# Kernel optimization log

Measured on AMD Instinct MI355X. Metric: run time of the kernel, lower is better.

The kernel has to match this reference:

```python
import jax, jax.numpy as jnp
import numpy as np

EMBED_DIM = 256
NUM_HEADS = 8
QUERY_HEAD_DIM = 24
BLOCK_SIZE = 8
IN_PROJ_DIM = 2 * QUERY_HEAD_DIM * NUM_HEADS  # 384


def _relative_position_index(bs: int) -> np.ndarray:
    coords = np.stack(np.meshgrid(np.arange(bs), np.arange(bs), indexing='ij'))  # (2, bs, bs)
    cf = coords.reshape(2, -1)                          # (2, bs^2)
    rel = cf[:, :, None] - cf[:, None, :]               # (2, bs^2, bs^2)
    rel = rel.transpose(1, 2, 0).astype(np.int32)       # (bs^2, bs^2, 2)
    rel[..., 0] += bs - 1
    rel[..., 1] += bs - 1
    rel[..., 0] *= 2 * bs - 1
    return rel.sum(-1)                                  # (bs^2, bs^2)


def setup_inputs() -> dict:
    key = jax.random.key(0)
    k1, k2, k3, k4, k5 = jax.random.split(key, 5)
    B, H, W, C = 2, 256, 256, EMBED_DIM
    num_tokens = H * W
    x = jax.random.normal(k1, (B, H, W, C), dtype=jnp.float32)
    reordered_indexes = jax.random.randint(k2, (1, num_tokens, 1), 0, num_tokens).astype(jnp.int64)
    # ScaledLinear: ordinary linear; initial_scale folded into weight magnitude
    scale = QUERY_HEAD_DIM ** (-0.25)
    w_in = jax.random.normal(k3, (EMBED_DIM, IN_PROJ_DIM), dtype=jnp.float32) * (scale / np.sqrt(EMBED_DIM))
    b_in = jax.random.normal(k4, (IN_PROJ_DIM,), dtype=jnp.float32) * 0.01
    n_rel = (2 * BLOCK_SIZE - 1) ** 2
    rel_bias_table = jax.random.uniform(k5, (n_rel, NUM_HEADS), dtype=jnp.float32) * 0.02
    rel_pos_index = jnp.asarray(_relative_position_index(BLOCK_SIZE), dtype=jnp.int32)
    return {"x": x, "reordered_indexes": reordered_indexes, "w_in": w_in,
            "b_in": b_in, "rel_bias_table": rel_bias_table, "rel_pos_index": rel_pos_index}


def reference(x, reordered_indexes, w_in, b_in, rel_bias_table, rel_pos_index):
    B, H, W, C = x.shape
    bs = BLOCK_SIZE
    nh = NUM_HEADS
    qhd = QUERY_HEAD_DIM
    nbh, nbw = H // bs, W // bs
    nbt = nbh * nbw
    num_tokens = H * W

    # optional token reordering (gather along token dim)
    idx = reordered_indexes[0, :, 0]                        # (num_tokens,)
    xf = x.reshape(B, num_tokens, C)[:, idx, :]             # (B, T, C)
    xf = xf.reshape(B, H, W, C)

    proj = xf @ w_in + b_in                                 # (B, H, W, 2*nh*qhd)
    qdim = qhd * nh
    query = proj[..., :qdim]
    key = proj[..., qdim:2 * qdim]  # whiten/balance are identity in eval math

    # window partition: (B, nbh, bs, nbw, bs, nh, qhd)
    q = query.reshape(B, nbh, bs, nbw, bs, nh, qhd)
    q = q.transpose(5, 0, 1, 3, 2, 4, 6).reshape(nh, B, nbt, bs * bs, qhd)
    k = key.reshape(B, nbh, bs, nbw, bs, nh, qhd)
    k = k.transpose(5, 0, 1, 3, 6, 2, 4).reshape(nh, B, nbt, qhd, bs * bs)

    attn_scores = jnp.matmul(q, k)                          # (nh, B, nbt, bs^2, bs^2)

    bias = rel_bias_table[rel_pos_index.reshape(-1)]        # (bs^2*bs^2, nh)
    bias = bias.reshape(bs * bs, bs * bs, nh).transpose(2, 0, 1)  # (nh, bs^2, bs^2)
    attn_scores = attn_scores + bias[:, None, None]

    return jax.nn.softmax(attn_scores, axis=-1)
```

## Files before the change

kernel.cpp:

```cpp
#include <hip/hip_runtime.h>

namespace {

typedef __attribute__((ext_vector_type(4))) float f32x4;
typedef __attribute__((ext_vector_type(8))) short bf16x8;

constexpr int WFRAG_ELEMS = 24 * 8 * 64 * 8;
constexpr int WFRAG_BYTES = WFRAG_ELEMS * 2;
constexpr int BIAS_ELEMS  = 8 * 64 * 64;
constexpr size_t WS_NEEDED = (size_t)WFRAG_BYTES + (size_t)BIAS_ELEMS * 4;

constexpr int TOK_OFF = 0;
constexpr int XS_OFF  = 256;
constexpr int CB_OFF  = 0;
constexpr int PB_OFF  = 49152;
constexpr int LDS_TOTAL = 65536;

__device__ __forceinline__ unsigned short f2bf(float f) {
  unsigned u = __float_as_uint(f);
  u += 0x7fffu + ((u >> 16) & 1u);
  return (unsigned short)(u >> 16);
}

__device__ __forceinline__ int cb_addr(int row, int col) {
  const int slot = (col >> 3) ^ (row & 7);
  return CB_OFF + row * 768 + (slot << 4) + ((col & 7) << 1);
}

__device__ __forceinline__ int pb_addr(int wavebase, int row16, int ktq) {
  return wavebase + row16 * 256 + (((ktq ^ row16) & 15) << 4);
}

__global__ void prep(const float* __restrict__ w_in,
                     const float* __restrict__ btab,
                     const int*   __restrict__ rpidx,
                     unsigned short* __restrict__ wfrag,
                     float* __restrict__ biasx) {
  const int t = blockIdx.x * 256 + threadIdx.x;
  if (t < WFRAG_ELEMS) {
    const int j    = t & 7;
    const int lane = (t >> 3) & 63;
    const int kk   = (t >> 9) & 7;
    const int nt   = t >> 12;
    const int k    = kk * 32 + (lane >> 4) * 8 + j;
    const int col  = nt * 16 + (lane & 15);
    wfrag[t] = f2bf(w_in[k * 384 + col]);
  } else if (t < WFRAG_ELEMS + BIAS_ELEMS) {
    const int o = t - WFRAG_ELEMS;
    const int j = o & 63, i = (o >> 6) & 63, h = o >> 12;
    biasx[o] = btab[rpidx[i * 64 + j] * 8 + h];
  }
}

template <bool USE_WS>
__global__ __launch_bounds__(256, 2)
void fused_mhaw(const float* __restrict__ x,
                const int*   __restrict__ reidx,
                const float* __restrict__ w_in,
                const float* __restrict__ b_in,
                const float* __restrict__ btab,
                const int*   __restrict__ rpidx,
                const unsigned short* __restrict__ wfrag,
                const float* __restrict__ biasx,
                float*       __restrict__ out) {
  extern __shared__ char lds[];
  int* tok           = reinterpret_cast<int*>(lds + TOK_OFF);
  unsigned short* xs = reinterpret_cast<unsigned short*>(lds + XS_OFF);

  const int tid  = threadIdx.x;
  const int b    = blockIdx.x >> 10;
  const int win  = blockIdx.x & 1023;
  const int wh   = win >> 5, ww = win & 31;
  const int wave = tid >> 6, lane = tid & 63;
  const int l15  = lane & 15, q = lane >> 4;
  const int pbase = PB_OFF + wave * 4096;

  if (tid < 64)
    tok[tid] = reidx[(wh * 8 + (tid >> 3)) * 256 + ww * 8 + (tid & 7)];
  __syncthreads();

  {
    const int srow = tid >> 2;
    const int part = tid & 3;
    const int sm_t = srow >> 4, sr15 = srow & 15;
    const int swr  = sr15 ^ (part << 1);
    const float* xrow = x + ((size_t)b * 65536 + (size_t)tok[srow]) * 256;
#pragma unroll
    for (int hf = 0; hf < 2; ++hf) {
      const float* src = xrow + hf * 128 + part * 32;
#pragma unroll
      for (int g = 0; g < 4; ++g) {
        const float4 v0 = *reinterpret_cast<const float4*>(src + g * 8);
        const float4 v1 = *reinterpret_cast<const float4*>(src + g * 8 + 4);
        bf16x8 u;
        u[0] = (short)f2bf(v0.x); u[1] = (short)f2bf(v0.y);
        u[2] = (short)f2bf(v0.z); u[3] = (short)f2bf(v0.w);
        u[4] = (short)f2bf(v1.x); u[5] = (short)f2bf(v1.y);
        u[6] = (short)f2bf(v1.z); u[7] = (short)f2bf(v1.w);
        *reinterpret_cast<bf16x8*>(
            xs + ((sm_t * 8 + hf * 4 + part) * 64 + g * 16 + swr) * 8) = u;
      }
    }
  }
  __syncthreads();

  f32x4 acc[6][4];
#pragma unroll
  for (int n = 0; n < 6; ++n)
#pragma unroll
    for (int m = 0; m < 4; ++m) acc[n][m] = (f32x4){0.f, 0.f, 0.f, 0.f};

#pragma unroll
  for (int kk = 0; kk < 8; ++kk) {
    const int rlane = q * 16 + (l15 ^ ((kk & 3) << 1));
    bf16x8 af[4];
#pragma unroll
    for (int m = 0; m < 4; ++m)
      af[m] = *reinterpret_cast<const bf16x8*>(xs + ((m * 8 + kk) * 64 + rlane) * 8);
#pragma unroll
    for (int n = 0; n < 6; ++n) {
      bf16x8 bfr;
      if (USE_WS) {
        bfr = *reinterpret_cast<const bf16x8*>(
            wfrag + (((wave * 6 + n) * 8 + kk) * 64 + lane) * 8);
      } else {
        const int colg = wave * 96 + n * 16 + l15;
#pragma unroll
        for (int jj = 0; jj < 8; ++jj)
          bfr[jj] = (short)f2bf(w_in[(kk * 32 + q * 8 + jj) * 384 + colg]);
      }
#pragma unroll
      for (int m = 0; m < 4; ++m)
        acc[n][m] = __builtin_amdgcn_mfma_f32_16x16x32_bf16(af[m], bfr, acc[n][m], 0, 0, 0);
    }
  }
  __syncthreads();

#pragma unroll
  for (int n = 0; n < 6; ++n) {
    const int colg = wave * 96 + n * 16 + l15;
    const float bv = b_in[colg];
#pragma unroll
    for (int m = 0; m < 4; ++m)
#pragma unroll
      for (int r = 0; r < 4; ++r) {
        const int row = m * 16 + q * 4 + r;
        *reinterpret_cast<unsigned short*>(lds + cb_addr(row, colg)) =
            f2bf(acc[n][m][r] + bv);
      }
  }
  __syncthreads();

  const bf16x8 vz = {0, 0, 0, 0, 0, 0, 0, 0};
  const f32x4 cz = {0.f, 0.f, 0.f, 0.f};

  for (int hh = 0; hh < 2; ++hh) {
    const int h = wave * 2 + hh;

    bf16x8 aq[4], bk[4];
#pragma unroll
    for (int mi = 0; mi < 4; ++mi)
      aq[mi] = (lane < 48)
                   ? *reinterpret_cast<const bf16x8*>(lds + cb_addr(mi * 16 + l15, h * 24 + q * 8))
                   : vz;
#pragma unroll
    for (int ni = 0; ni < 4; ++ni)
      bk[ni] = (lane < 48)
                   ? *reinterpret_cast<const bf16x8*>(lds + cb_addr(ni * 16 + l15, 192 + h * 24 + q * 8))
                   : vz;

    f32x4 s[4][4];
#pragma unroll
    for (int ai = 0; ai < 4; ++ai)
#pragma unroll
      for (int bi = 0; bi < 4; ++bi)
        s[ai][bi] = __builtin_amdgcn_mfma_f32_16x16x32_bf16(bk[ai], aq[bi], cz, 0, 0, 0);

    const size_t obase = (((size_t)h * 2 + b) * 1024 + win) * 4096;

#pragma unroll
    for (int bi = 0; bi < 4; ++bi) {
      const int qt = bi * 16 + l15;
      f32x4 p[4];
#pragma unroll
      for (int ai = 0; ai < 4; ++ai) {
        if (USE_WS) {
          const f32x4 bb = *reinterpret_cast<const f32x4*>(
              biasx + ((size_t)(h * 64 + qt)) * 64 + ai * 16 + q * 4);
          p[ai] = s[ai][bi] + bb;
        } else {
#pragma unroll
          for (int r = 0; r < 4; ++r)
            p[ai][r] = s[ai][bi][r] +
                       btab[rpidx[qt * 64 + ai * 16 + q * 4 + r] * 8 + h];
        }
      }
      float mx = fmaxf(fmaxf(p[0][0], p[0][1]), fmaxf(p[0][2], p[0][3]));
#pragma unroll
      for (int ai = 1; ai < 4; ++ai)
        mx = fmaxf(mx, fmaxf(fmaxf(p[ai][0], p[ai][1]), fmaxf(p[ai][2], p[ai][3])));
      mx = fmaxf(mx, __shfl_xor(mx, 16));
      mx = fmaxf(mx, __shfl_xor(mx, 32));

      float sum = 0.f;
#pragma unroll
      for (int ai = 0; ai < 4; ++ai)
#pragma unroll
        for (int r = 0; r < 4; ++r) {
          p[ai][r] = __expf(p[ai][r] - mx);
          sum += p[ai][r];
        }
      sum += __shfl_xor(sum, 16);
      sum += __shfl_xor(sum, 32);
      const float inv = __builtin_amdgcn_rcpf(sum);

#pragma unroll
      for (int ai = 0; ai < 4; ++ai) {
        const f32x4 o = p[ai] * inv;
        *reinterpret_cast<f32x4*>(lds + pb_addr(pbase, l15, ai * 4 + q)) = o;
      }
#pragma unroll
      for (int i = 0; i < 4; ++i) {
        const int row16 = i * 4 + q;
        const f32x4 v = *reinterpret_cast<const f32x4*>(
            lds + pb_addr(pbase, row16, l15));
        __builtin_nontemporal_store(
            v, reinterpret_cast<f32x4*>(
                   out + obase + (size_t)(bi * 16 + row16) * 64 + l15 * 4));
      }
    }
  }
}

}

extern "C" void kernel_launch(void* const* d_in, const int* in_sizes, int n_in,
                              void* d_out, int out_size, void* d_ws, size_t ws_size,
                              hipStream_t stream) {
  const float* x     = (const float*)d_in[0];
  const int*   reidx = (const int*)d_in[1];
  const float* w_in  = (const float*)d_in[2];
  const float* b_in  = (const float*)d_in[3];
  const float* btab  = (const float*)d_in[4];
  const int*   rpidx = (const int*)d_in[5];
  float* out = (float*)d_out;

  const bool use_ws = ws_size >= WS_NEEDED;
  unsigned short* wfrag = (unsigned short*)d_ws;
  float* biasx = (float*)((char*)d_ws + WFRAG_BYTES);

  if (use_ws) {
    prep<<<dim3((WFRAG_ELEMS + BIAS_ELEMS + 255) / 256), dim3(256), 0, stream>>>(
        w_in, btab, rpidx, wfrag, biasx);
    fused_mhaw<true><<<dim3(2048), dim3(256), LDS_TOTAL, stream>>>(
        x, reidx, w_in, b_in, btab, rpidx, wfrag, biasx, out);
  } else {
    fused_mhaw<false><<<dim3(2048), dim3(256), LDS_TOTAL, stream>>>(
        x, reidx, w_in, b_in, btab, rpidx, nullptr, nullptr, out);
  }
}
```

Before: 125.2 us.

## Shrink LDS footprint to raise occupancy by reusing projection buffer for softmax staging

LDS is cut from 64KB to 48KB: the token index table is dropped (each thread loads its own reidx value) and the per-wave softmax staging buffer now overlays the projection buffer once both heads' Q/K fragments have been read into registers and a barrier has passed. Launch bounds are raised to 3 blocks per CU so more windows can be resident. The risk is extra register pressure from holding the second head's fragments and the first head's scores at once, which could cause spills under the tighter register budget.

```diff
diff --git a/kernel.cpp b/kernel.cpp
--- a/kernel.cpp
+++ b/kernel.cpp
@@ -10,11 +10,10 @@
 constexpr int BIAS_ELEMS  = 8 * 64 * 64;
 constexpr size_t WS_NEEDED = (size_t)WFRAG_BYTES + (size_t)BIAS_ELEMS * 4;
 
-constexpr int TOK_OFF = 0;
-constexpr int XS_OFF  = 256;
-constexpr int CB_OFF  = 0;
-constexpr int PB_OFF  = 49152;
-constexpr int LDS_TOTAL = 65536;
+constexpr int XS_OFF    = 0;
+constexpr int CB_OFF    = 0;
+constexpr int PB_STRIDE = 4096;
+constexpr int LDS_TOTAL = 49152;
 
 __device__ __forceinline__ unsigned short f2bf(float f) {
   unsigned u = __float_as_uint(f);
@@ -53,7 +52,7 @@
 }
 
 template <bool USE_WS>
-__global__ __launch_bounds__(256, 2)
+__global__ __launch_bounds__(256, 3)
 void fused_mhaw(const float* __restrict__ x,
                 const int*   __restrict__ reidx,
                 const float* __restrict__ w_in,
@@ -64,7 +63,6 @@
                 const float* __restrict__ biasx,
                 float*       __restrict__ out) {
   extern __shared__ char lds[];
-  int* tok           = reinterpret_cast<int*>(lds + TOK_OFF);
   unsigned short* xs = reinterpret_cast<unsigned short*>(lds + XS_OFF);
 
   const int tid  = threadIdx.x;
@@ -73,18 +71,15 @@
   const int wh   = win >> 5, ww = win & 31;
   const int wave = tid >> 6, lane = tid & 63;
   const int l15  = lane & 15, q = lane >> 4;
-  const int pbase = PB_OFF + wave * 4096;
-
-  if (tid < 64)
-    tok[tid] = reidx[(wh * 8 + (tid >> 3)) * 256 + ww * 8 + (tid & 7)];
-  __syncthreads();
+  const int pbase = wave * PB_STRIDE;
 
   {
     const int srow = tid >> 2;
     const int part = tid & 3;
     const int sm_t = srow >> 4, sr15 = srow & 15;
     const int swr  = sr15 ^ (part << 1);
-    const float* xrow = x + ((size_t)b * 65536 + (size_t)tok[srow]) * 256;
+    const int tokv = reidx[(wh * 8 + (srow >> 3)) * 256 + ww * 8 + (srow & 7)];
+    const float* xrow = x + ((size_t)b * 65536 + (size_t)tokv) * 256;
 #pragma unroll
     for (int hf = 0; hf < 2; ++hf) {
       const float* src = xrow + hf * 128 + part * 32;
@@ -153,31 +148,10 @@
 
   const bf16x8 vz = {0, 0, 0, 0, 0, 0, 0, 0};
   const f32x4 cz = {0.f, 0.f, 0.f, 0.f};
-
-  for (int hh = 0; hh < 2; ++hh) {
-    const int h = wave * 2 + hh;
-
-    bf16x8 aq[4], bk[4];
-#pragma unroll
-    for (int mi = 0; mi < 4; ++mi)
-      aq[mi] = (lane < 48)
-                   ? *reinterpret_cast<const bf16x8*>(lds + cb_addr(mi * 16 + l15, h * 24 + q * 8))
-                   : vz;
-#pragma unroll
-    for (int ni = 0; ni < 4; ++ni)
-      bk[ni] = (lane < 48)
-                   ? *reinterpret_cast<const bf16x8*>(lds + cb_addr(ni * 16 + l15, 192 + h * 24 + q * 8))
-                   : vz;
-
-    f32x4 s[4][4];
-#pragma unroll
-    for (int ai = 0; ai < 4; ++ai)
-#pragma unroll
-      for (int bi = 0; bi < 4; ++bi)
-        s[ai][bi] = __builtin_amdgcn_mfma_f32_16x16x32_bf16(bk[ai], aq[bi], cz, 0, 0, 0);
-
+  const int h0 = wave * 2, h1 = h0 + 1;
+
+  auto softmax_store = [&](int h, f32x4 (&s)[4][4]) {
     const size_t obase = (((size_t)h * 2 + b) * 1024 + win) * 4096;
-
 #pragma unroll
     for (int bi = 0; bi < 4; ++bi) {
       const int qt = bi * 16 + l15;
@@ -229,7 +203,52 @@
                    out + obase + (size_t)(bi * 16 + row16) * 64 + l15 * 4));
       }
     }
-  }
+  };
+
+  f32x4 s0t[4][4];
+  {
+    bf16x8 aq[4], bk[4];
+#pragma unroll
+    for (int mi = 0; mi < 4; ++mi)
+      aq[mi] = (lane < 48)
+                   ? *reinterpret_cast<const bf16x8*>(lds + cb_addr(mi * 16 + l15, h0 * 24 + q * 8))
+                   : vz;
+#pragma unroll
+    for (int ni = 0; ni < 4; ++ni)
+      bk[ni] = (lane < 48)
+                   ? *reinterpret_cast<const bf16x8*>(lds + cb_addr(ni * 16 + l15, 192 + h0 * 24 + q * 8))
+                   : vz;
+#pragma unroll
+    for (int ai = 0; ai < 4; ++ai)
+#pragma unroll
+      for (int bi = 0; bi < 4; ++bi)
+        s0t[ai][bi] = __builtin_amdgcn_mfma_f32_16x16x32_bf16(bk[ai], aq[bi], cz, 0, 0, 0);
+  }
+
+  bf16x8 aq1[4], bk1[4];
+#pragma unroll
+  for (int mi = 0; mi < 4; ++mi)
+    aq1[mi] = (lane < 48)
+                  ? *reinterpret_cast<const bf16x8*>(lds + cb_addr(mi * 16 + l15, h1 * 24 + q * 8))
+                  : vz;
+#pragma unroll
+  for (int ni = 0; ni < 4; ++ni)
+    bk1[ni] = (lane < 48)
+                  ? *reinterpret_cast<const bf16x8*>(lds + cb_addr(ni * 16 + l15, 192 + h1 * 24 + q * 8))
+                  : vz;
+
+  __syncthreads();
+
+  softmax_store(h0, s0t);
+
+  f32x4 s1t[4][4];
+#pragma unroll
+  for (int ai = 0; ai < 4; ++ai)
+#pragma unroll
+    for (int bi = 0; bi < 4; ++bi)
+      s1t[ai][bi] = __builtin_amdgcn_mfma_f32_16x16x32_bf16(bk1[ai], aq1[bi], cz, 0, 0, 0);
+
+  softmax_store(h1, s1t);
 }
 
 }
```

Measured after the change: 110.3 us. 1.13x faster.

## Give each wave its own Q/K heads and halve LDS for higher occupancy

Applied to the files above, without the earlier changes.

Changes the projection column assignment so each wave computes the query and key columns for its own two heads, which removes the block-wide combined buffer and the second block barrier. LDS per block drops to 32 KB with per-wave scratch regions, and launch bounds are raised to 4 blocks per CU. Token indices are loaded directly per thread, so the tok LDS staging and its barrier are gone, and the QK MFMAs are computed per query tile to cut live registers. The risk is register spilling under the tighter bound, plus reused scratch that depends on the added waitcnt and sched barrier for correctness.

```diff
diff --git a/kernel.cpp b/kernel.cpp
--- a/kernel.cpp
+++ b/kernel.cpp
@@ -10,11 +10,7 @@
 constexpr int BIAS_ELEMS  = 8 * 64 * 64;
 constexpr size_t WS_NEEDED = (size_t)WFRAG_BYTES + (size_t)BIAS_ELEMS * 4;
 
-constexpr int TOK_OFF = 0;
-constexpr int XS_OFF  = 256;
-constexpr int CB_OFF  = 0;
-constexpr int PB_OFF  = 49152;
-constexpr int LDS_TOTAL = 65536;
+constexpr int LDS_TOTAL = 32768;
 
 __device__ __forceinline__ unsigned short f2bf(float f) {
   unsigned u = __float_as_uint(f);
@@ -22,13 +18,12 @@
   return (unsigned short)(u >> 16);
 }
 
-__device__ __forceinline__ int cb_addr(int row, int col) {
-  const int slot = (col >> 3) ^ (row & 7);
-  return CB_OFF + row * 768 + (slot << 4) + ((col & 7) << 1);
-}
-
-__device__ __forceinline__ int pb_addr(int wavebase, int row16, int ktq) {
-  return wavebase + row16 * 256 + (((ktq ^ row16) & 15) << 4);
+__device__ __forceinline__ int cbw_addr(int wbase, int row, int c) {
+  return wbase + row * 128 + ((((c >> 3) ^ (row & 7)) & 7) << 4) + ((c & 7) << 1);
+}
+
+__device__ __forceinline__ int pb_addr(int pbase, int row16, int ktq) {
+  return pbase + row16 * 256 + (((ktq ^ row16) & 15) << 4);
 }
 
 __global__ void prep(const float* __restrict__ w_in,
@@ -53,7 +48,7 @@
 }
 
 template <bool USE_WS>
-__global__ __launch_bounds__(256, 2)
+__global__ __launch_bounds__(256, 4)
 void fused_mhaw(const float* __restrict__ x,
                 const int*   __restrict__ reidx,
                 const float* __restrict__ w_in,
@@ -64,8 +59,7 @@
                 const float* __restrict__ biasx,
                 float*       __restrict__ out) {
   extern __shared__ char lds[];
-  int* tok           = reinterpret_cast<int*>(lds + TOK_OFF);
-  unsigned short* xs = reinterpret_cast<unsigned short*>(lds + XS_OFF);
+  unsigned short* xs = reinterpret_cast<unsigned short*>(lds);
 
   const int tid  = threadIdx.x;
   const int b    = blockIdx.x >> 10;
@@ -73,18 +67,16 @@
   const int wh   = win >> 5, ww = win & 31;
   const int wave = tid >> 6, lane = tid & 63;
   const int l15  = lane & 15, q = lane >> 4;
-  const int pbase = PB_OFF + wave * 4096;
-
-  if (tid < 64)
-    tok[tid] = reidx[(wh * 8 + (tid >> 3)) * 256 + ww * 8 + (tid & 7)];
-  __syncthreads();
+  const int wbase = wave * 8192;
+  const int pbase = wbase + 4096;
 
   {
     const int srow = tid >> 2;
     const int part = tid & 3;
     const int sm_t = srow >> 4, sr15 = srow & 15;
     const int swr  = sr15 ^ (part << 1);
-    const float* xrow = x + ((size_t)b * 65536 + (size_t)tok[srow]) * 256;
+    const int tokv = reidx[(wh * 8 + (srow >> 3)) * 256 + ww * 8 + (srow & 7)];
+    const float* xrow = x + ((size_t)b * 65536 + (size_t)tokv) * 256;
 #pragma unroll
     for (int hf = 0; hf < 2; ++hf) {
       const float* src = xrow + hf * 128 + part * 32;
@@ -119,12 +111,13 @@
       af[m] = *reinterpret_cast<const bf16x8*>(xs + ((m * 8 + kk) * 64 + rlane) * 8);
 #pragma unroll
     for (int n = 0; n < 6; ++n) {
+      const int nt = (n < 3) ? (3 * wave + n) : (12 + 3 * wave + (n - 3));
       bf16x8 bfr;
       if (USE_WS) {
         bfr = *reinterpret_cast<const bf16x8*>(
-            wfrag + (((wave * 6 + n) * 8 + kk) * 64 + lane) * 8);
+            wfrag + (((size_t)nt * 8 + kk) * 64 + lane) * 8);
       } else {
-        const int colg = wave * 96 + n * 16 + l15;
+        const int colg = nt * 16 + l15;
 #pragma unroll
         for (int jj = 0; jj < 8; ++jj)
           bfr[jj] = (short)f2bf(w_in[(kk * 32 + q * 8 + jj) * 384 + colg]);
@@ -136,63 +129,73 @@
   }
   __syncthreads();
 
-#pragma unroll
-  for (int n = 0; n < 6; ++n) {
-    const int colg = wave * 96 + n * 16 + l15;
-    const float bv = b_in[colg];
-#pragma unroll
-    for (int m = 0; m < 4; ++m)
-#pragma unroll
-      for (int r = 0; r < 4; ++r) {
-        const int row = m * 16 + q * 4 + r;
-        *reinterpret_cast<unsigned short*>(lds + cb_addr(row, colg)) =
-            f2bf(acc[n][m][r] + bv);
-      }
-  }
-  __syncthreads();
-
   const bf16x8 vz = {0, 0, 0, 0, 0, 0, 0, 0};
   const f32x4 cz = {0.f, 0.f, 0.f, 0.f};
 
-  for (int hh = 0; hh < 2; ++hh) {
-    const int h = wave * 2 + hh;
-
-    bf16x8 aq[4], bk[4];
-#pragma unroll
-    for (int mi = 0; mi < 4; ++mi)
-      aq[mi] = (lane < 48)
-                   ? *reinterpret_cast<const bf16x8*>(lds + cb_addr(mi * 16 + l15, h * 24 + q * 8))
+#pragma unroll
+  for (int hl = 0; hl < 2; ++hl) {
+    const int h = 2 * wave + hl;
+
+#pragma unroll
+    for (int n = 0; n < 6; ++n) {
+      const int nt = (n < 3) ? (3 * wave + n) : (12 + 3 * wave + (n - 3));
+      const int wc = (n % 3) * 16 + l15;
+      const bool act = (wc >= hl * 24) && (wc < hl * 24 + 24);
+      const int c = (n < 3 ? 0 : 24) + wc - hl * 24;
+      const float bv = b_in[nt * 16 + l15];
+      if (act) {
+#pragma unroll
+        for (int m = 0; m < 4; ++m)
+#pragma unroll
+          for (int r = 0; r < 4; ++r) {
+            const int row = m * 16 + q * 4 + r;
+            *reinterpret_cast<unsigned short*>(lds + cbw_addr(wbase, row, c)) =
+                f2bf(acc[n][m][r] + bv);
+          }
+      }
+    }
+
+    bf16x8 bk[4], aqhi[2];
+#pragma unroll
+    for (int ai = 0; ai < 4; ++ai)
+      bk[ai] = (lane < 48)
+                   ? *reinterpret_cast<const bf16x8*>(
+                         lds + cbw_addr(wbase, ai * 16 + l15, 24 + q * 8))
                    : vz;
 #pragma unroll
-    for (int ni = 0; ni < 4; ++ni)
-      bk[ni] = (lane < 48)
-                   ? *reinterpret_cast<const bf16x8*>(lds + cb_addr(ni * 16 + l15, 192 + h * 24 + q * 8))
-                   : vz;
-
-    f32x4 s[4][4];
-#pragma unroll
-    for (int ai = 0; ai < 4; ++ai)
-#pragma unroll
-      for (int bi = 0; bi < 4; ++bi)
-        s[ai][bi] = __builtin_amdgcn_mfma_f32_16x16x32_bf16(bk[ai], aq[bi], cz, 0, 0, 0);
+    for (int i = 0; i < 2; ++i)
+      aqhi[i] = (lane < 48)
+                    ? *reinterpret_cast<const bf16x8*>(
+                          lds + cbw_addr(wbase, (2 + i) * 16 + l15, q * 8))
+                    : vz;
 
     const size_t obase = (((size_t)h * 2 + b) * 1024 + win) * 4096;
 
 #pragma unroll
     for (int bi = 0; bi < 4; ++bi) {
+      const bf16x8 aqv =
+          (bi < 2) ? ((lane < 48)
+                          ? *reinterpret_cast<const bf16x8*>(
+                                lds + cbw_addr(wbase, bi * 16 + l15, q * 8))
+                          : vz)
+                   : aqhi[bi - 2];
+
+      f32x4 p[4];
+#pragma unroll
+      for (int ai = 0; ai < 4; ++ai)
+        p[ai] = __builtin_amdgcn_mfma_f32_16x16x32_bf16(bk[ai], aqv, cz, 0, 0, 0);
+
       const int qt = bi * 16 + l15;
-      f32x4 p[4];
 #pragma unroll
       for (int ai = 0; ai < 4; ++ai) {
         if (USE_WS) {
           const f32x4 bb = *reinterpret_cast<const f32x4*>(
               biasx + ((size_t)(h * 64 + qt)) * 64 + ai * 16 + q * 4);
-          p[ai] = s[ai][bi] + bb;
+          p[ai] += bb;
         } else {
 #pragma unroll
           for (int r = 0; r < 4; ++r)
-            p[ai][r] = s[ai][bi][r] +
-                       btab[rpidx[qt * 64 + ai * 16 + q * 4 + r] * 8 + h];
+            p[ai][r] += btab[rpidx[qt * 64 + ai * 16 + q * 4 + r] * 8 + h];
         }
       }
       float mx = fmaxf(fmaxf(p[0][0], p[0][1]), fmaxf(p[0][2], p[0][3]));
@@ -229,6 +232,9 @@
                    out + obase + (size_t)(bi * 16 + row16) * 64 + l15 * 4));
       }
     }
+
+    asm volatile("s_waitcnt lgkmcnt(0)" ::: "memory");
+    __builtin_amdgcn_sched_barrier(0);
   }
 }
 
```

Measured after the change: 187.5 us. +49.8%, slower.
